# Performance work log

Measured on AMD Instinct MI355X. Metric: run time of the kernel, lower is better.

Reference implementation:

```python
import jax, jax.numpy as jnp
import numpy as np

QUERY_DIM = 192
KEY_DIM = 64
DIM_OUT = 128
C = QUERY_DIM + KEY_DIM  # 256
N = 10000
E = 320000
M = 5000


def setup_inputs() -> dict:
    key = jax.random.key(0)
    ks = jax.random.split(key, 16)
    s = 1.0 / np.sqrt(C)
    inp = {
        "query": jax.random.normal(ks[0], (N, QUERY_DIM), jnp.float32),
        "key_idx": jax.random.randint(ks[1], (N,), 0, KEY_DIM),
        "edge_index": jax.random.randint(ks[2], (2, E), 0, N),
        "mask_idx": jnp.sort(jax.random.randint(ks[3], (M,), 0, N)),
        "Wq": jax.random.normal(ks[4], (C, C), jnp.float32) * s,
        "bq": jnp.zeros((C,), jnp.float32),
        "Wk": jax.random.normal(ks[5], (C, C), jnp.float32) * s,
        "bk": jnp.zeros((C,), jnp.float32),
        "Wv": jax.random.normal(ks[6], (C, C), jnp.float32) * s,
        "bv": jnp.zeros((C,), jnp.float32),
        "Ws": jax.random.normal(ks[7], (C, C), jnp.float32) * s,
        "bs": jnp.zeros((C,), jnp.float32),
        "Wo": jax.random.normal(ks[8], (KEY_DIM, DIM_OUT), jnp.float32) * (1.0 / np.sqrt(KEY_DIM)),
        "bo": jnp.zeros((DIM_OUT,), jnp.float32),
    }
    return inp


def reference(query, key_idx, edge_index, mask_idx, Wq, bq, Wk, bk, Wv, bv, Ws, bs, Wo, bo):
    # node features: [N, C] = concat(query, one_hot(key))
    x = jnp.concatenate([query, jax.nn.one_hot(key_idx, KEY_DIM, dtype=query.dtype)], axis=1)
    src, dst = edge_index[0], edge_index[1]  # messages flow src -> dst
    # node-level projections (dense GEMMs), then edge gather
    q_n = x @ Wq + bq
    k_n = x @ Wk + bk
    v_n = x @ Wv + bv
    q = q_n[dst]  # [E, C]
    k = k_n[src]
    v = v_n[src]
    score = jnp.sum(q * k, axis=-1) / jnp.sqrt(jnp.asarray(C, x.dtype))  # [E]
    # per-destination softmax over incoming edges
    m = jax.ops.segment_max(score, dst, num_segments=N)  # [N]
    m = jnp.where(jnp.isfinite(m), m, 0.0)
    e = jnp.exp(score - m[dst])
    denom = jax.ops.segment_sum(e, dst, num_segments=N)
    alpha = e / (denom[dst] + 1e-16)
    # scatter-aggregate weighted values + root/skip connection
    agg = jax.ops.segment_sum(alpha[:, None] * v, dst, num_segments=N)  # [N, C]
    out = agg + (x @ Ws + bs)
    h = jax.nn.relu(out[mask_idx])  # [M, C]
    h = h[:, QUERY_DIM:]  # [M, KEY_DIM]
    return h @ Wo + bo  # [M, DIM_OUT]
```

## Files before the change

### kernel.cpp

```cpp
#include <hip/hip_runtime.h>

#define QDIM 192
#define KDIM 64
#define CDIM 256
#define DOUT 128
#define CAP 128
#define NEG_INF __int_as_float(0xFF800000)
#define LDP 200

typedef _Float16 hf2 __attribute__((ext_vector_type(2)));
typedef _Float16 half4 __attribute__((ext_vector_type(4)));
typedef _Float16 half8 __attribute__((ext_vector_type(8)));
typedef float floatx4 __attribute__((ext_vector_type(4)));

#if defined(__has_builtin)
#if __has_builtin(__builtin_amdgcn_fdot2)
#define HAVE_FDOT2 1
#endif
#endif

__device__ __forceinline__ hf2 bc_h2(unsigned u) { return __builtin_bit_cast(hf2, u); }

__device__ __forceinline__ float dot2acc(hf2 a, hf2 b, float c) {
#ifdef HAVE_FDOT2
    return __builtin_amdgcn_fdot2(a, b, c, false);
#else
    return c + (float)a[0] * (float)b[0] + (float)a[1] * (float)b[1];
#endif
}

__device__ __forceinline__ void wmap(int j, const float* Wq, const float* Wk,
                                     const float* Wv, const float* Ws,
                                     const float** W, int* wcol) {
    if (j < 256)      { *W = Wq; *wcol = j; }
    else if (j < 512) { *W = Wk; *wcol = j - 256; }
    else if (j < 576) { *W = Wv; *wcol = QDIM + (j - 512); }
    else              { *W = Ws; *wcol = QDIM + (j - 576); }
}

__global__ __launch_bounds__(256) void gemm_nodes(
        const float* __restrict__ query, const int* __restrict__ key_idx,
        const float* Wq, const float* bq, const float* Wk, const float* bk,
        const float* Wv, const float* bv, const float* Ws, const float* bs,
        const int* __restrict__ mask, int M, unsigned char* __restrict__ mrk,
        _Float16* __restrict__ Qbuf, _Float16* __restrict__ Kbuf,
        _Float16* __restrict__ Vbuf, float* __restrict__ Sbuf, int N) {
    __shared__ __align__(16) _Float16 As[64 * LDP];
    __shared__ __align__(16) _Float16 Bs[64 * LDP];
    int bm = blockIdx.x * 64;
    int bn = blockIdx.y * 64;
    int tid = threadIdx.x;

    int gid = (blockIdx.y * gridDim.x + blockIdx.x) * 256 + tid;
    if (gid < M) mrk[mask[gid]] = 1;

    #pragma unroll
    for (int it = 0; it < 12; it++) {
        int idx = tid + it * 256;
        int r = idx / 48, f4 = idx % 48;
        int gr = bm + r;
        float4 va = make_float4(0.f, 0.f, 0.f, 0.f);
        if (gr < N) va = ((const float4*)(query + (size_t)gr * QDIM))[f4];
        half4 h = { (_Float16)va.x, (_Float16)va.y, (_Float16)va.z, (_Float16)va.w };
        *((half4*)&As[r * LDP + f4 * 4]) = h;
    }
    {
        int cj = tid >> 2;
        int ks = (tid & 3) * 48;
        const float* W; int wc;
        wmap(bn + cj, Wq, Wk, Wv, Ws, &W, &wc);
        #pragma unroll 8
        for (int k = 0; k < 48; k++)
            Bs[cj * LDP + ks + k] = (_Float16)W[(ks + k) * CDIM + wc];
    }
    __syncthreads();

    int w = tid >> 6, l = tid & 63;
    int lrow = l & 15, quad = l >> 4;
    floatx4 acc[4] = {{0.f,0.f,0.f,0.f},{0.f,0.f,0.f,0.f},{0.f,0.f,0.f,0.f},{0.f,0.f,0.f,0.f}};

    const _Float16* arow = &As[(w * 16 + lrow) * LDP + quad * 8];
    #pragma unroll
    for (int ks = 0; ks < 6; ks++) {
        half8 af = *(const half8*)(arow + ks * 32);
        #pragma unroll
        for (int nt = 0; nt < 4; nt++) {
            half8 bf = *(const half8*)(&Bs[(nt * 16 + lrow) * LDP + quad * 8 + ks * 32]);
            acc[nt] = __builtin_amdgcn_mfma_f32_16x16x32_f16(af, bf, acc[nt], 0, 0, 0);
        }
    }

    int ki[4];
    #pragma unroll
    for (int reg = 0; reg < 4; reg++) {
        int gr = bm + w * 16 + quad * 4 + reg;
        ki[reg] = (gr < N) ? key_idx[gr] : 0;
    }
    #pragma unroll
    for (int nt = 0; nt < 4; nt++) {
        int gc = bn + nt * 16 + lrow;
        const float* W; int wc;
        wmap(gc, Wq, Wk, Wv, Ws, &W, &wc);
        const float* bvec = (gc < 256) ? bq : (gc < 512) ? bk : (gc < 576) ? bv : bs;
        float bias = bvec[wc];
        #pragma unroll
        for (int reg = 0; reg < 4; reg++) {
            int gr = bm + w * 16 + quad * 4 + reg;
            if (gr < N) {
                float v = acc[nt][reg] + W[(QDIM + ki[reg]) * CDIM + wc] + bias;
                if (gc < 256)      Qbuf[(size_t)gr * 256 + gc] = (_Float16)v;
                else if (gc < 512) Kbuf[(size_t)gr * 256 + (gc - 256)] = (_Float16)v;
                else if (gc < 576) Vbuf[(size_t)gr * KDIM + (gc - 512)] = (_Float16)v;
                else               Sbuf[(size_t)gr * KDIM + (gc - 576)] = v;
            }
        }
    }
}

__global__ __launch_bounds__(256) void scatter_kernel(
        const int* __restrict__ src, const int* __restrict__ dst,
        const unsigned char* __restrict__ mrk,
        int* __restrict__ deg, int* __restrict__ adj, int E) {
    int e = blockIdx.x * blockDim.x + threadIdx.x;
    if (e < E) {
        int d = dst[e];
        if (mrk[d]) {
            int slot = atomicAdd(&deg[d], 1);
            if (slot < CAP) adj[d * CAP + slot] = src[e];
        }
    }
}

__global__ __launch_bounds__(256) void attend_out(
        const _Float16* __restrict__ Qbuf, const _Float16* __restrict__ Kbuf,
        const _Float16* __restrict__ Vbuf, const float* __restrict__ Sbuf,
        const int* __restrict__ deg, const int* __restrict__ adj,
        const int* __restrict__ mask, const float* __restrict__ Wo,
        const float* __restrict__ bo, float* __restrict__ out, int M) {
    int w = threadIdx.x >> 6, lane = threadIdx.x & 63;
    int r = blockIdx.x * 4 + w;
    if (r >= M) return;
    int node = mask[r];
    if (r > 0 && mask[r - 1] == node) return;
    int l = lane & 15, g = lane >> 4;

    const uint4* qp = (const uint4*)(Qbuf + (size_t)node * 256 + l * 16);
    uint4 qa = qp[0], qb = qp[1];
    hf2 qh[8] = { bc_h2(qa.x), bc_h2(qa.y), bc_h2(qa.z), bc_h2(qa.w),
                  bc_h2(qb.x), bc_h2(qb.y), bc_h2(qb.z), bc_h2(qb.w) };

    int dn = min(deg[node], CAP);
    const int* arow = adj + (size_t)node * CAP;

    float m = NEG_INF, dsum = 0.f;
    float a0 = 0.f, a1 = 0.f, a2 = 0.f, a3 = 0.f;
    for (int i = g; i < dn; i += 4) {
        int s = arow[i];
        const uint4* kp = (const uint4*)(Kbuf + (size_t)s * 256 + l * 16);
        uint4 ka = kp[0], kb = kp[1];
        float d = 0.f;
        d = dot2acc(bc_h2(ka.x), qh[0], d);
        d = dot2acc(bc_h2(ka.y), qh[1], d);
        d = dot2acc(bc_h2(ka.z), qh[2], d);
        d = dot2acc(bc_h2(ka.w), qh[3], d);
        d = dot2acc(bc_h2(kb.x), qh[4], d);
        d = dot2acc(bc_h2(kb.y), qh[5], d);
        d = dot2acc(bc_h2(kb.z), qh[6], d);
        d = dot2acc(bc_h2(kb.w), qh[7], d);
        d += __shfl_xor(d, 1, 64);
        d += __shfl_xor(d, 2, 64);
        d += __shfl_xor(d, 4, 64);
        d += __shfl_xor(d, 8, 64);
        float sc = d * 0.0625f;
        float m_new = fmaxf(m, sc);
        float scale = __expf(m - m_new);
        float p = __expf(sc - m_new);
        dsum = dsum * scale + p;
        uint2 vv = *(const uint2*)(Vbuf + (size_t)s * KDIM + l * 4);
        hf2 v01 = bc_h2(vv.x), v23 = bc_h2(vv.y);
        a0 = a0 * scale + p * (float)v01[0];
        a1 = a1 * scale + p * (float)v01[1];
        a2 = a2 * scale + p * (float)v23[0];
        a3 = a3 * scale + p * (float)v23[1];
        m = m_new;
    }

    float Mx = fmaxf(m, __shfl_xor(m, 16, 64));
    Mx = fmaxf(Mx, __shfl_xor(Mx, 32, 64));
    float wgt = __expf(m - Mx);
    if (m == NEG_INF) wgt = 0.f;
    float ds = dsum * wgt;
    ds += __shfl_xor(ds, 16, 64);
    ds += __shfl_xor(ds, 32, 64);
    a0 *= wgt; a1 *= wgt; a2 *= wgt; a3 *= wgt;
    a0 += __shfl_xor(a0, 16, 64); a0 += __shfl_xor(a0, 32, 64);
    a1 += __shfl_xor(a1, 16, 64); a1 += __shfl_xor(a1, 32, 64);
    a2 += __shfl_xor(a2, 16, 64); a2 += __shfl_xor(a2, 32, 64);
    a3 += __shfl_xor(a3, 16, 64); a3 += __shfl_xor(a3, 32, 64);
    float inv = 1.f / (ds + 1e-16f);

    float4 s4 = *((const float4*)(Sbuf + (size_t)node * KDIM + l * 4));
    float h0 = fmaxf(a0 * inv + s4.x, 0.f);
    float h1 = fmaxf(a1 * inv + s4.y, 0.f);
    float h2 = fmaxf(a2 * inv + s4.z, 0.f);
    float h3 = fmaxf(a3 * inv + s4.w, 0.f);

    float o0 = bo[lane], o1 = bo[lane + 64];
    #pragma unroll
    for (int c = 0; c < KDIM; c++) {
        float hc = (c & 3) == 0 ? h0 : (c & 3) == 1 ? h1 : (c & 3) == 2 ? h2 : h3;
        float hv = __shfl(hc, c >> 2, 64);
        o0 += hv * Wo[c * DOUT + lane];
        o1 += hv * Wo[c * DOUT + 64 + lane];
    }
    int rr = r;
    do {
        out[(size_t)rr * DOUT + lane] = o0;
        out[(size_t)rr * DOUT + 64 + lane] = o1;
        rr++;
    } while (rr < M && mask[rr] == node);
}

extern "C" void kernel_launch(void* const* d_in, const int* in_sizes, int n_in,
                              void* d_out, int out_size, void* d_ws, size_t ws_size,
                              hipStream_t stream) {
    const float* query    = (const float*)d_in[0];
    const int* key_idx    = (const int*)d_in[1];
    const int* edge_index = (const int*)d_in[2];
    const int* mask_idx   = (const int*)d_in[3];
    const float* Wq = (const float*)d_in[4];
    const float* bq = (const float*)d_in[5];
    const float* Wk = (const float*)d_in[6];
    const float* bk = (const float*)d_in[7];
    const float* Wv = (const float*)d_in[8];
    const float* bv = (const float*)d_in[9];
    const float* Ws = (const float*)d_in[10];
    const float* bs = (const float*)d_in[11];
    const float* Wo = (const float*)d_in[12];
    const float* bo = (const float*)d_in[13];

    int N = in_sizes[0] / QDIM;
    int E = in_sizes[2] / 2;
    int M = in_sizes[3];
    const int* esrc = edge_index;
    const int* edst = edge_index + E;

    char* wsb = (char*)d_ws;
    size_t off = 0;
    auto alloc = [&](size_t nbytes) { char* p = wsb + off; off += (nbytes + 15) & ~15ull; return p; };
    _Float16* Qbuf = (_Float16*)alloc((size_t)N * 256 * 2);
    _Float16* Kbuf = (_Float16*)alloc((size_t)N * 256 * 2);
    _Float16* Vbuf = (_Float16*)alloc((size_t)N * KDIM * 2);
    float* Sbuf    = (float*)alloc((size_t)N * KDIM * 4);
    int*   deg     = (int*)alloc((size_t)N * 4 + (size_t)N);
    unsigned char* mrk = (unsigned char*)(deg + N);
    int*   adj     = (int*)alloc((size_t)N * CAP * 4);

    hipMemsetAsync(deg, 0, (size_t)N * 5, stream);

    dim3 ggrid((N + 63) / 64, 10);
    gemm_nodes<<<ggrid, 256, 0, stream>>>(query, key_idx, Wq, bq, Wk, bk, Wv, bv,
                                          Ws, bs, mask_idx, M, mrk,
                                          Qbuf, Kbuf, Vbuf, Sbuf, N);

    scatter_kernel<<<(E + 255) / 256, 256, 0, stream>>>(esrc, edst, mrk, deg, adj, E);

    attend_out<<<(M + 3) / 4, 256, 0, stream>>>(Qbuf, Kbuf, Vbuf, Sbuf, deg, adj,
                                                mask_idx, Wo, bo, (float*)d_out, M);
}
```

Measured before the change: 152.1 us.

## Coalesce weight staging, fold mask marking into degree sentinel, widen attention lanes

The GEMM weight tile is now loaded with threads spread across columns, so global reads are coalesced, and the column-to-matrix mapping is resolved once per block. The separate mask byte array is dropped: degrees are memset to a large negative sentinel and masked nodes are reset to zero, so the scatter kernel does an unconditional atomic and keeps only non-negative slots. The attention kernel uses 8 lanes per edge instead of 16, with wider K and V loads per lane, so each wave processes 8 edges at once. The trade-off is atomics on every edge, including unmasked destinations, in exchange for removing the byte-array load and branch.

```diff
diff --git a/kernel.cpp b/kernel.cpp
--- a/kernel.cpp
+++ b/kernel.cpp
@@ -29,20 +29,11 @@
 #endif
 }
 
-__device__ __forceinline__ void wmap(int j, const float* Wq, const float* Wk,
-                                     const float* Wv, const float* Ws,
-                                     const float** W, int* wcol) {
-    if (j < 256)      { *W = Wq; *wcol = j; }
-    else if (j < 512) { *W = Wk; *wcol = j - 256; }
-    else if (j < 576) { *W = Wv; *wcol = QDIM + (j - 512); }
-    else              { *W = Ws; *wcol = QDIM + (j - 576); }
-}
-
 __global__ __launch_bounds__(256) void gemm_nodes(
         const float* __restrict__ query, const int* __restrict__ key_idx,
         const float* Wq, const float* bq, const float* Wk, const float* bk,
         const float* Wv, const float* bv, const float* Ws, const float* bs,
-        const int* __restrict__ mask, int M, unsigned char* __restrict__ mrk,
+        const int* __restrict__ mask, int M, int* __restrict__ deg,
         _Float16* __restrict__ Qbuf, _Float16* __restrict__ Kbuf,
         _Float16* __restrict__ Vbuf, float* __restrict__ Sbuf, int N) {
     __shared__ __align__(16) _Float16 As[64 * LDP];
@@ -52,7 +43,13 @@
     int tid = threadIdx.x;
 
     int gid = (blockIdx.y * gridDim.x + blockIdx.x) * 256 + tid;
-    if (gid < M) mrk[mask[gid]] = 1;
+    if (gid < M) deg[mask[gid]] = 0;
+
+    const float* Wb; const float* bvec; int wc0;
+    if (bn < 256)      { Wb = Wq; bvec = bq; wc0 = bn; }
+    else if (bn < 512) { Wb = Wk; bvec = bk; wc0 = bn - 256; }
+    else if (bn < 576) { Wb = Wv; bvec = bv; wc0 = QDIM + (bn - 512); }
+    else               { Wb = Ws; bvec = bs; wc0 = QDIM + (bn - 576); }
 
     #pragma unroll
     for (int it = 0; it < 12; it++) {
@@ -65,13 +62,18 @@
         *((half4*)&As[r * LDP + f4 * 4]) = h;
     }
     {
-        int cj = tid >> 2;
-        int ks = (tid & 3) * 48;
-        const float* W; int wc;
-        wmap(bn + cj, Wq, Wk, Wv, Ws, &W, &wc);
-        #pragma unroll 8
-        for (int k = 0; k < 48; k++)
-            Bs[cj * LDP + ks + k] = (_Float16)W[(ks + k) * CDIM + wc];
+        int c = tid & 63, r0 = tid >> 6;
+        #pragma unroll
+        for (int it = 0; it < 6; it++) {
+            int kg = r0 + it * 4;
+            float f[8];
+            #pragma unroll
+            for (int j = 0; j < 8; j++)
+                f[j] = Wb[(size_t)(kg * 8 + j) * CDIM + wc0 + c];
+            half8 h8 = { (_Float16)f[0], (_Float16)f[1], (_Float16)f[2], (_Float16)f[3],
+                         (_Float16)f[4], (_Float16)f[5], (_Float16)f[6], (_Float16)f[7] };
+            *((half8*)&Bs[c * LDP + kg * 8]) = h8;
+        }
     }
     __syncthreads();
 
@@ -99,15 +101,13 @@
     #pragma unroll
     for (int nt = 0; nt < 4; nt++) {
         int gc = bn + nt * 16 + lrow;
-        const float* W; int wc;
-        wmap(gc, Wq, Wk, Wv, Ws, &W, &wc);
-        const float* bvec = (gc < 256) ? bq : (gc < 512) ? bk : (gc < 576) ? bv : bs;
+        int wc = wc0 + nt * 16 + lrow;
         float bias = bvec[wc];
         #pragma unroll
         for (int reg = 0; reg < 4; reg++) {
             int gr = bm + w * 16 + quad * 4 + reg;
             if (gr < N) {
-                float v = acc[nt][reg] + W[(QDIM + ki[reg]) * CDIM + wc] + bias;
+                float v = acc[nt][reg] + Wb[(size_t)(QDIM + ki[reg]) * CDIM + wc] + bias;
                 if (gc < 256)      Qbuf[(size_t)gr * 256 + gc] = (_Float16)v;
                 else if (gc < 512) Kbuf[(size_t)gr * 256 + (gc - 256)] = (_Float16)v;
                 else if (gc < 576) Vbuf[(size_t)gr * KDIM + (gc - 512)] = (_Float16)v;
@@ -119,15 +119,12 @@
 
 __global__ __launch_bounds__(256) void scatter_kernel(
         const int* __restrict__ src, const int* __restrict__ dst,
-        const unsigned char* __restrict__ mrk,
         int* __restrict__ deg, int* __restrict__ adj, int E) {
     int e = blockIdx.x * blockDim.x + threadIdx.x;
     if (e < E) {
         int d = dst[e];
-        if (mrk[d]) {
-            int slot = atomicAdd(&deg[d], 1);
-            if (slot < CAP) adj[d * CAP + slot] = src[e];
-        }
+        int slot = atomicAdd(&deg[d], 1);
+        if ((unsigned)slot < CAP) adj[d * CAP + slot] = src[e];
     }
 }
 
@@ -142,74 +139,89 @@
     if (r >= M) return;
     int node = mask[r];
     if (r > 0 && mask[r - 1] == node) return;
-    int l = lane & 15, g = lane >> 4;
-
-    const uint4* qp = (const uint4*)(Qbuf + (size_t)node * 256 + l * 16);
-    uint4 qa = qp[0], qb = qp[1];
-    hf2 qh[8] = { bc_h2(qa.x), bc_h2(qa.y), bc_h2(qa.z), bc_h2(qa.w),
-                  bc_h2(qb.x), bc_h2(qb.y), bc_h2(qb.z), bc_h2(qb.w) };
+    int l = lane & 7, g = lane >> 3;
+
+    const uint4* qp = (const uint4*)(Qbuf + (size_t)node * 256 + l * 32);
+    uint4 q0 = qp[0], q1 = qp[1], q2 = qp[2], q3 = qp[3];
+    hf2 qh[16] = { bc_h2(q0.x), bc_h2(q0.y), bc_h2(q0.z), bc_h2(q0.w),
+                   bc_h2(q1.x), bc_h2(q1.y), bc_h2(q1.z), bc_h2(q1.w),
+                   bc_h2(q2.x), bc_h2(q2.y), bc_h2(q2.z), bc_h2(q2.w),
+                   bc_h2(q3.x), bc_h2(q3.y), bc_h2(q3.z), bc_h2(q3.w) };
 
     int dn = min(deg[node], CAP);
     const int* arow = adj + (size_t)node * CAP;
 
     float m = NEG_INF, dsum = 0.f;
-    float a0 = 0.f, a1 = 0.f, a2 = 0.f, a3 = 0.f;
-    for (int i = g; i < dn; i += 4) {
+    float acc[8] = {0.f, 0.f, 0.f, 0.f, 0.f, 0.f, 0.f, 0.f};
+    for (int i = g; i < dn; i += 8) {
         int s = arow[i];
-        const uint4* kp = (const uint4*)(Kbuf + (size_t)s * 256 + l * 16);
-        uint4 ka = kp[0], kb = kp[1];
+        const uint4* kp = (const uint4*)(Kbuf + (size_t)s * 256 + l * 32);
+        uint4 k0 = kp[0], k1 = kp[1], k2 = kp[2], k3 = kp[3];
+        uint4 vv = *(const uint4*)(Vbuf + (size_t)s * KDIM + l * 8);
         float d = 0.f;
-        d = dot2acc(bc_h2(ka.x), qh[0], d);
-        d = dot2acc(bc_h2(ka.y), qh[1], d);
-        d = dot2acc(bc_h2(ka.z), qh[2], d);
-        d = dot2acc(bc_h2(ka.w), qh[3], d);
-        d = dot2acc(bc_h2(kb.x), qh[4], d);
-        d = dot2acc(bc_h2(kb.y), qh[5], d);
-        d = dot2acc(bc_h2(kb.z), qh[6], d);
-        d = dot2acc(bc_h2(kb.w), qh[7], d);
+        d = dot2acc(bc_h2(k0.x), qh[0], d);  d = dot2acc(bc_h2(k0.y), qh[1], d);
+        d = dot2acc(bc_h2(k0.z), qh[2], d);  d = dot2acc(bc_h2(k0.w), qh[3], d);
+        d = dot2acc(bc_h2(k1.x), qh[4], d);  d = dot2acc(bc_h2(k1.y), qh[5], d);
+        d = dot2acc(bc_h2(k1.z), qh[6], d);  d = dot2acc(bc_h2(k1.w), qh[7], d);
+        d = dot2acc(bc_h2(k2.x), qh[8], d);  d = dot2acc(bc_h2(k2.y), qh[9], d);
+        d = dot2acc(bc_h2(k2.z), qh[10], d); d = dot2acc(bc_h2(k2.w), qh[11], d);
+        d = dot2acc(bc_h2(k3.x), qh[12], d); d = dot2acc(bc_h2(k3.y), qh[13], d);
+        d = dot2acc(bc_h2(k3.z), qh[14], d); d = dot2acc(bc_h2(k3.w), qh[15], d);
         d += __shfl_xor(d, 1, 64);
         d += __shfl_xor(d, 2, 64);
         d += __shfl_xor(d, 4, 64);
-        d += __shfl_xor(d, 8, 64);
         float sc = d * 0.0625f;
         float m_new = fmaxf(m, sc);
         float scale = __expf(m - m_new);
         float p = __expf(sc - m_new);
         dsum = dsum * scale + p;
-        uint2 vv = *(const uint2*)(Vbuf + (size_t)s * KDIM + l * 4);
-        hf2 v01 = bc_h2(vv.x), v23 = bc_h2(vv.y);
-        a0 = a0 * scale + p * (float)v01[0];
-        a1 = a1 * scale + p * (float)v01[1];
-        a2 = a2 * scale + p * (float)v23[0];
-        a3 = a3 * scale + p * (float)v23[1];
+        hf2 v01 = bc_h2(vv.x), v23 = bc_h2(vv.y), v45 = bc_h2(vv.z), v67 = bc_h2(vv.w);
+        acc[0] = acc[0] * scale + p * (float)v01[0];
+        acc[1] = acc[1] * scale + p * (float)v01[1];
+        acc[2] = acc[2] * scale + p * (float)v23[0];
+        acc[3] = acc[3] * scale + p * (float)v23[1];
+        acc[4] = acc[4] * scale + p * (float)v45[0];
+        acc[5] = acc[5] * scale + p * (float)v45[1];
+        acc[6] = acc[6] * scale + p * (float)v67[0];
+        acc[7] = acc[7] * scale + p * (float)v67[1];
         m = m_new;
     }
 
-    float Mx = fmaxf(m, __shfl_xor(m, 16, 64));
+    float Mx = m;
+    Mx = fmaxf(Mx, __shfl_xor(Mx, 8, 64));
+    Mx = fmaxf(Mx, __shfl_xor(Mx, 16, 64));
     Mx = fmaxf(Mx, __shfl_xor(Mx, 32, 64));
-    float wgt = __expf(m - Mx);
-    if (m == NEG_INF) wgt = 0.f;
+    float wgt = (m == NEG_INF) ? 0.f : __expf(m - Mx);
     float ds = dsum * wgt;
+    ds += __shfl_xor(ds, 8, 64);
     ds += __shfl_xor(ds, 16, 64);
     ds += __shfl_xor(ds, 32, 64);
-    a0 *= wgt; a1 *= wgt; a2 *= wgt; a3 *= wgt;
-    a0 += __shfl_xor(a0, 16, 64); a0 += __shfl_xor(a0, 32, 64);
-    a1 += __shfl_xor(a1, 16, 64); a1 += __shfl_xor(a1, 32, 64);
-    a2 += __shfl_xor(a2, 16, 64); a2 += __shfl_xor(a2, 32, 64);
-    a3 += __shfl_xor(a3, 16, 64); a3 += __shfl_xor(a3, 32, 64);
+    #pragma unroll
+    for (int j = 0; j < 8; j++) {
+        float a = acc[j] * wgt;
+        a += __shfl_xor(a, 8, 64);
+        a += __shfl_xor(a, 16, 64);
+        a += __shfl_xor(a, 32, 64);
+        acc[j] = a;
+    }
     float inv = 1.f / (ds + 1e-16f);
 
-    float4 s4 = *((const float4*)(Sbuf + (size_t)node * KDIM + l * 4));
-    float h0 = fmaxf(a0 * inv + s4.x, 0.f);
-    float h1 = fmaxf(a1 * inv + s4.y, 0.f);
-    float h2 = fmaxf(a2 * inv + s4.z, 0.f);
-    float h3 = fmaxf(a3 * inv + s4.w, 0.f);
+    float4 s0 = *((const float4*)(Sbuf + (size_t)node * KDIM + l * 8));
+    float4 s1 = *((const float4*)(Sbuf + (size_t)node * KDIM + l * 8 + 4));
+    float h[8];
+    h[0] = fmaxf(acc[0] * inv + s0.x, 0.f);
+    h[1] = fmaxf(acc[1] * inv + s0.y, 0.f);
+    h[2] = fmaxf(acc[2] * inv + s0.z, 0.f);
+    h[3] = fmaxf(acc[3] * inv + s0.w, 0.f);
+    h[4] = fmaxf(acc[4] * inv + s1.x, 0.f);
+    h[5] = fmaxf(acc[5] * inv + s1.y, 0.f);
+    h[6] = fmaxf(acc[6] * inv + s1.z, 0.f);
+    h[7] = fmaxf(acc[7] * inv + s1.w, 0.f);
 
     float o0 = bo[lane], o1 = bo[lane + 64];
     #pragma unroll
     for (int c = 0; c < KDIM; c++) {
-        float hc = (c & 3) == 0 ? h0 : (c & 3) == 1 ? h1 : (c & 3) == 2 ? h2 : h3;
-        float hv = __shfl(hc, c >> 2, 64);
+        float hv = __shfl(h[c & 7], c >> 3, 64);
         o0 += hv * Wo[c * DOUT + lane];
         o1 += hv * Wo[c * DOUT + 64 + lane];
     }
@@ -252,18 +264,17 @@
     _Float16* Kbuf = (_Float16*)alloc((size_t)N * 256 * 2);
     _Float16* Vbuf = (_Float16*)alloc((size_t)N * KDIM * 2);
     float* Sbuf    = (float*)alloc((size_t)N * KDIM * 4);
-    int*   deg     = (int*)alloc((size_t)N * 4 + (size_t)N);
-    unsigned char* mrk = (unsigned char*)(deg + N);
+    int*   deg     = (int*)alloc((size_t)N * 4);
     int*   adj     = (int*)alloc((size_t)N * CAP * 4);
 
-    hipMemsetAsync(deg, 0, (size_t)N * 5, stream);
+    hipMemsetAsync(deg, 0x80, (size_t)N * 4, stream);
 
     dim3 ggrid((N + 63) / 64, 10);
     gemm_nodes<<<ggrid, 256, 0, stream>>>(query, key_idx, Wq, bq, Wk, bk, Wv, bv,
-                                          Ws, bs, mask_idx, M, mrk,
+                                          Ws, bs, mask_idx, M, deg,
                                           Qbuf, Kbuf, Vbuf, Sbuf, N);
 
-    scatter_kernel<<<(E + 255) / 256, 256, 0, stream>>>(esrc, edst, mrk, deg, adj, E);
+    scatter_kernel<<<(E + 255) / 256, 256, 0, stream>>>(esrc, edst, deg, adj, E);
 
     attend_out<<<(M + 3) / 4, 256, 0, stream>>>(Qbuf, Kbuf, Vbuf, Sbuf, deg, adj,
                                                 mask_idx, Wo, bo, (float*)d_out, M);
```

Result: slower. 157.5 us (+3.5%).

## Pre-convert query to fp16 once, coalesce weight tile loads, fold mask into deg

Applied to the files above, without the earlier changes.

A prep kernel converts query to fp16 once, so the ten column blocks of the GEMM no longer each reread and convert the fp32 rows. It also initializes deg to INT_MIN, replacing the memset, and the GEMM sets deg to zero for masked nodes, so the separate marker array and its load in the scatter disappear. Unmasked destinations then get negative atomic slots, which an unsigned compare rejects. The weight tile load now reads rows coalesced across columns and writes half8 vectors, and the per-column weight/bias selection is hoisted per block. The cost is an extra kernel launch and an extra fp16 buffer, and scatter now performs atomics on every edge instead of only masked ones.

```diff
diff --git a/kernel.cpp b/kernel.cpp
--- a/kernel.cpp
+++ b/kernel.cpp
@@ -29,20 +29,25 @@
 #endif
 }
 
-__device__ __forceinline__ void wmap(int j, const float* Wq, const float* Wk,
-                                     const float* Wv, const float* Ws,
-                                     const float** W, int* wcol) {
-    if (j < 256)      { *W = Wq; *wcol = j; }
-    else if (j < 512) { *W = Wk; *wcol = j - 256; }
-    else if (j < 576) { *W = Wv; *wcol = QDIM + (j - 512); }
-    else              { *W = Ws; *wcol = QDIM + (j - 576); }
+__global__ __launch_bounds__(256) void prep_kernel(
+        const float* __restrict__ query, _Float16* __restrict__ Qh,
+        int* __restrict__ deg, int qchunks, int N) {
+    int t = blockIdx.x * blockDim.x + threadIdx.x;
+    if (t < qchunks) {
+        float4 v = ((const float4*)query)[t];
+        half4 h = { (_Float16)v.x, (_Float16)v.y, (_Float16)v.z, (_Float16)v.w };
+        ((half4*)Qh)[t] = h;
+        return;
+    }
+    t -= qchunks;
+    if (t < N) deg[t] = (int)0x80000000;
 }
 
 __global__ __launch_bounds__(256) void gemm_nodes(
-        const float* __restrict__ query, const int* __restrict__ key_idx,
+        const _Float16* __restrict__ Qh, const int* __restrict__ key_idx,
         const float* Wq, const float* bq, const float* Wk, const float* bk,
         const float* Wv, const float* bv, const float* Ws, const float* bs,
-        const int* __restrict__ mask, int M, unsigned char* __restrict__ mrk,
+        const int* __restrict__ mask, int M, int* __restrict__ deg,
         _Float16* __restrict__ Qbuf, _Float16* __restrict__ Kbuf,
         _Float16* __restrict__ Vbuf, float* __restrict__ Sbuf, int N) {
     __shared__ __align__(16) _Float16 As[64 * LDP];
@@ -52,26 +57,36 @@
     int tid = threadIdx.x;
 
     int gid = (blockIdx.y * gridDim.x + blockIdx.x) * 256 + tid;
-    if (gid < M) mrk[mask[gid]] = 1;
-
-    #pragma unroll
-    for (int it = 0; it < 12; it++) {
+    if (gid < M) deg[mask[gid]] = 0;
+
+    const float* Wb; const float* bvec; int wc0;
+    if (bn < 256)      { Wb = Wq; bvec = bq; wc0 = bn; }
+    else if (bn < 512) { Wb = Wk; bvec = bk; wc0 = bn - 256; }
+    else if (bn < 576) { Wb = Wv; bvec = bv; wc0 = QDIM + (bn - 512); }
+    else               { Wb = Ws; bvec = bs; wc0 = QDIM + (bn - 576); }
+
+    #pragma unroll
+    for (int it = 0; it < 6; it++) {
         int idx = tid + it * 256;
-        int r = idx / 48, f4 = idx % 48;
+        int r = idx / 24, q4 = idx % 24;
         int gr = bm + r;
-        float4 va = make_float4(0.f, 0.f, 0.f, 0.f);
-        if (gr < N) va = ((const float4*)(query + (size_t)gr * QDIM))[f4];
-        half4 h = { (_Float16)va.x, (_Float16)va.y, (_Float16)va.z, (_Float16)va.w };
-        *((half4*)&As[r * LDP + f4 * 4]) = h;
+        uint4 va = make_uint4(0u, 0u, 0u, 0u);
+        if (gr < N) va = ((const uint4*)(Qh + (size_t)gr * QDIM))[q4];
+        *((uint4*)&As[r * LDP + q4 * 8]) = va;
     }
     {
-        int cj = tid >> 2;
-        int ks = (tid & 3) * 48;
-        const float* W; int wc;
-        wmap(bn + cj, Wq, Wk, Wv, Ws, &W, &wc);
-        #pragma unroll 8
-        for (int k = 0; k < 48; k++)
-            Bs[cj * LDP + ks + k] = (_Float16)W[(ks + k) * CDIM + wc];
+        int c = tid & 63, r0 = tid >> 6;
+        #pragma unroll
+        for (int it = 0; it < 6; it++) {
+            int kg = r0 + it * 4;
+            float f[8];
+            #pragma unroll
+            for (int j = 0; j < 8; j++)
+                f[j] = Wb[(size_t)(kg * 8 + j) * CDIM + wc0 + c];
+            half8 h8 = { (_Float16)f[0], (_Float16)f[1], (_Float16)f[2], (_Float16)f[3],
+                         (_Float16)f[4], (_Float16)f[5], (_Float16)f[6], (_Float16)f[7] };
+            *((half8*)&Bs[c * LDP + kg * 8]) = h8;
+        }
     }
     __syncthreads();
 
@@ -99,15 +114,13 @@
     #pragma unroll
     for (int nt = 0; nt < 4; nt++) {
         int gc = bn + nt * 16 + lrow;
-        const float* W; int wc;
-        wmap(gc, Wq, Wk, Wv, Ws, &W, &wc);
-        const float* bvec = (gc < 256) ? bq : (gc < 512) ? bk : (gc < 576) ? bv : bs;
+        int wc = wc0 + nt * 16 + lrow;
         float bias = bvec[wc];
         #pragma unroll
         for (int reg = 0; reg < 4; reg++) {
             int gr = bm + w * 16 + quad * 4 + reg;
             if (gr < N) {
-                float v = acc[nt][reg] + W[(QDIM + ki[reg]) * CDIM + wc] + bias;
+                float v = acc[nt][reg] + Wb[(size_t)(QDIM + ki[reg]) * CDIM + wc] + bias;
                 if (gc < 256)      Qbuf[(size_t)gr * 256 + gc] = (_Float16)v;
                 else if (gc < 512) Kbuf[(size_t)gr * 256 + (gc - 256)] = (_Float16)v;
                 else if (gc < 576) Vbuf[(size_t)gr * KDIM + (gc - 512)] = (_Float16)v;
@@ -119,15 +132,12 @@
 
 __global__ __launch_bounds__(256) void scatter_kernel(
         const int* __restrict__ src, const int* __restrict__ dst,
-        const unsigned char* __restrict__ mrk,
         int* __restrict__ deg, int* __restrict__ adj, int E) {
     int e = blockIdx.x * blockDim.x + threadIdx.x;
     if (e < E) {
         int d = dst[e];
-        if (mrk[d]) {
-            int slot = atomicAdd(&deg[d], 1);
-            if (slot < CAP) adj[d * CAP + slot] = src[e];
-        }
+        int slot = atomicAdd(&deg[d], 1);
+        if ((unsigned)slot < CAP) adj[d * CAP + slot] = src[e];
     }
 }
 
@@ -187,8 +197,7 @@
 
     float Mx = fmaxf(m, __shfl_xor(m, 16, 64));
     Mx = fmaxf(Mx, __shfl_xor(Mx, 32, 64));
-    float wgt = __expf(m - Mx);
-    if (m == NEG_INF) wgt = 0.f;
+    float wgt = (m == NEG_INF) ? 0.f : __expf(m - Mx);
     float ds = dsum * wgt;
     ds += __shfl_xor(ds, 16, 64);
     ds += __shfl_xor(ds, 32, 64);
@@ -248,22 +257,23 @@
     char* wsb = (char*)d_ws;
     size_t off = 0;
     auto alloc = [&](size_t nbytes) { char* p = wsb + off; off += (nbytes + 15) & ~15ull; return p; };
+    _Float16* Qh   = (_Float16*)alloc((size_t)N * QDIM * 2);
     _Float16* Qbuf = (_Float16*)alloc((size_t)N * 256 * 2);
     _Float16* Kbuf = (_Float16*)alloc((size_t)N * 256 * 2);
     _Float16* Vbuf = (_Float16*)alloc((size_t)N * KDIM * 2);
     float* Sbuf    = (float*)alloc((size_t)N * KDIM * 4);
-    int*   deg     = (int*)alloc((size_t)N * 4 + (size_t)N);
-    unsigned char* mrk = (unsigned char*)(deg + N);
+    int*   deg     = (int*)alloc((size_t)N * 4);
     int*   adj     = (int*)alloc((size_t)N * CAP * 4);
 
-    hipMemsetAsync(deg, 0, (size_t)N * 5, stream);
+    int qchunks = N * QDIM / 4;
+    prep_kernel<<<(qchunks + N + 255) / 256, 256, 0, stream>>>(query, Qh, deg, qchunks, N);
 
     dim3 ggrid((N + 63) / 64, 10);
-    gemm_nodes<<<ggrid, 256, 0, stream>>>(query, key_idx, Wq, bq, Wk, bk, Wv, bv,
-                                          Ws, bs, mask_idx, M, mrk,
+    gemm_nodes<<<ggrid, 256, 0, stream>>>(Qh, key_idx, Wq, bq, Wk, bk, Wv, bv,
+                                          Ws, bs, mask_idx, M, deg,
                                           Qbuf, Kbuf, Vbuf, Sbuf, N);
 
-    scatter_kernel<<<(E + 255) / 256, 256, 0, stream>>>(esrc, edst, mrk, deg, adj, E);
+    scatter_kernel<<<(E + 255) / 256, 256, 0, stream>>>(esrc, edst, deg, adj, E);
 
     attend_out<<<(M + 3) / 4, 256, 0, stream>>>(Qbuf, Kbuf, Vbuf, Sbuf, deg, adj,
                                                 mask_idx, Wo, bo, (float*)d_out, M);
```

New measurement: 148.4 us. -2.4%, faster.
